# Kernel tuning notes

Hardware: AMD Instinct MI355X
Metric: run time of the kernel (lower is better)

## Reference

```python
import jax, jax.numpy as jnp
import numpy as np

BETA = 0.95
THR = 0.8
SLOPE = 25.0  # fast_sigmoid surrogate slope


@jax.custom_vjp
def spike(x):
    # Heaviside forward, fast-sigmoid surrogate backward (snntorch surrogate.fast_sigmoid)
    return (x > 0).astype(x.dtype)

def _spike_fwd(x):
    return spike(x), x

def _spike_bwd(x, g):
    return (g / (SLOPE * jnp.abs(x) + 1.0) ** 2,)

spike.defvjp(_spike_fwd, _spike_bwd)


def setup_inputs() -> dict:
    key = jax.random.key(0)
    k1, k2, k3 = jax.random.split(key, 3)
    B, T, D, H, C = 512, 2000, 20, 128, 10
    x = jax.random.normal(k1, (B, T, D), dtype=jnp.float32)
    # kaiming_normal_ with nonlinearity='linear': std = 1/sqrt(fan_in)
    W1 = jax.random.normal(k2, (H, D), dtype=jnp.float32) / np.sqrt(D)
    b1 = jnp.zeros((H,), jnp.float32)
    W2 = jax.random.normal(k3, (C, H), dtype=jnp.float32) / np.sqrt(H)
    b2 = jnp.zeros((C,), jnp.float32)
    return {"x": x, "W1": W1, "b1": b1, "W2": W2, "b2": b2}


def reference(x, W1, b1, W2, b2):
    B, T, D = x.shape
    H = W1.shape[0]

    def step(mem, xt):
        cur = xt @ W1.T + b1                                  # [B,H]
        # snntorch Leaky: reset based on PREVIOUS mem (detached), subtract mechanism
        reset = jax.lax.stop_gradient(spike(mem - THR))
        mem_new = BETA * mem + cur - reset * THR
        spk = spike(mem_new - THR)
        return mem_new, spk

    mem0 = jnp.zeros((B, H), x.dtype)
    _, spks = jax.lax.scan(step, mem0, jnp.swapaxes(x, 0, 1))  # spks: [T,B,H]

    spikeCounts = spks.sum(0)                                  # [B,H]
    # sum_t fc2(spk_t) = spikeCounts @ W2^T + T * b2
    logits = (spikeCounts @ W2.T + T * b2) / T
    logits = logits + 0.1 * ((spikeCounts / (T + 1e-6)) @ W2.T + b2)
    return logits
```

## Files before the change

kernel.cpp:

```cpp
#include <hip/hip_runtime.h>
#include <stdint.h>

#define Bdim 512
#define Tdim 2000
#define Ddim 20
#define Hdim 128
#define Cdim 10
#define TT   64
#define NCH  32
#define BETA 0.95f
#define THR  0.8f

typedef float f32x2 __attribute__((ext_vector_type(2)));
typedef float f32x4 __attribute__((ext_vector_type(4)));
typedef int   i32x4 __attribute__((ext_vector_type(4)));

#define CVT_HILO(HI, LO, F0, F1) {                                                     \
    asm volatile("v_cvt_pk_bf16_f32 %0, %1, %2" : "=v"(HI) : "v"(F0), "v"(F1));        \
    const float h0f_ = __uint_as_float((HI) << 16);                                    \
    const float h1f_ = __uint_as_float((HI) & 0xFFFF0000u);                            \
    const float l0_ = (F0) - h0f_;  const float l1_ = (F1) - h1f_;                     \
    asm volatile("v_cvt_pk_bf16_f32 %0, %1, %2" : "=v"(LO) : "v"(l0_), "v"(l1_)); }

#define MFMA0(ACC, A8, B8) \
  asm volatile("v_mfma_f32_16x16x32_bf16 %0, %1, %2, 0"  : "=v"(ACC) : "v"(A8), "v"(B8));
#define MFMA(ACC, A8, B8)  \
  asm volatile("v_mfma_f32_16x16x32_bf16 %0, %1, %2, %0" : "+v"(ACC) : "v"(A8), "v"(B8));

__global__ __launch_bounds__(256, 1) void snn_spec2_kernel(
    const float* __restrict__ x,
    const float* __restrict__ W1,
    const float* __restrict__ b1,
    const float* __restrict__ W2,
    const float* __restrict__ b2,
    float* __restrict__ out)
{
  const int b   = blockIdx.x;
  const int tid = threadIdx.x;
  const int wid = tid >> 6;
  const int l   = tid & 63;
  const int r   = l & 15;
  const int g   = l >> 4;

  __shared__ __align__(16) float xraw[2][TT * Ddim];
  __shared__ __align__(16) float cur[2][TT * 132];
  __shared__ float cnt_s[Hdim];

  const float* xb = x + (size_t)b * (Tdim * Ddim);
  const float* const clampMax = x + (size_t)Bdim * Tdim * Ddim - 4;

  const uint32_t xrawB = (uint32_t)(uintptr_t)&xraw[0][0];
  const uint32_t curB  = (uint32_t)(uintptr_t)&cur[0][0];

  i32x4 bhi[8], blo[8];
  f32x4 zero4, ovr;
  bool  sel23 = false, g3f = false;
  if (wid < 2) {
    const bool g2 = (g == 2);
    g3f   = (g == 3);
    sel23 = g2 | g3f;
    zero4[0]=0.f; zero4[1]=0.f; zero4[2]=0.f; zero4[3]=0.f;
    ovr = zero4; if (g2) ovr[0] = 1.0f;
#pragma unroll
    for (int ni = 0; ni < 8; ++ni) {
      const int hh = ni * 16 + r;
      float wv[8];
#pragma unroll
      for (int j = 0; j < 8; ++j) {
        const int k = 8 * g + j;
        wv[j] = (k < Ddim) ? W1[hh * Ddim + k] : ((k == Ddim) ? b1[hh] : 0.0f);
      }
#pragma unroll
      for (int d = 0; d < 4; ++d) {
        const uint32_t u0 = __float_as_uint(wv[2*d]), u1 = __float_as_uint(wv[2*d+1]);
        const uint32_t h0 = (u0 + 0x8000u) & 0xFFFF0000u;
        const uint32_t h1 = (u1 + 0x8000u) & 0xFFFF0000u;
        bhi[ni][d] = (int)(h1 | (h0 >> 16));
        const float l0 = wv[2*d]   - __uint_as_float(h0);
        const float l1 = wv[2*d+1] - __uint_as_float(h1);
        const uint32_t e0 = (__float_as_uint(l0) + 0x8000u) & 0xFFFF0000u;
        const uint32_t e1 = (__float_as_uint(l1) + 0x8000u) & 0xFFFF0000u;
        blo[ni][d] = (int)(e1 | (e0 >> 16));
      }
    }
  }

  float    mem = 0.0f;
  bool     sp  = false;
  uint32_t cnt = 0u;
  f32x2    negT2; negT2[0] = -THR; negT2[1] = -THR;
  const int sid = wid - 2;

#define STAGE(CH, BUF) do {                                                            \
    const float* g0_ = xb + (CH) * 1280 + wid * 640 + l * 4;                           \
    char* lb_ = (char*)&xraw[0][0] + (BUF) * 5120 + wid * 2560 + l * 16;               \
    const float* p0_ = g0_;        if (p0_ > clampMax) p0_ = clampMax;                 \
    const float* p1_ = g0_ + 256;  if (p1_ > clampMax) p1_ = clampMax;                 \
    __builtin_amdgcn_global_load_lds(                                                  \
      (const __attribute__((address_space(1))) unsigned int*)p0_,                      \
      (__attribute__((address_space(3))) unsigned int*)lb_, 16, 0, 0);                 \
    __builtin_amdgcn_global_load_lds(                                                  \
      (const __attribute__((address_space(1))) unsigned int*)p1_,                      \
      (__attribute__((address_space(3))) unsigned int*)(lb_ + 1024), 16, 0, 0);        \
    if (l < 32) {                                                                      \
      const float* p2_ = g0_ + 512;  if (p2_ > clampMax) p2_ = clampMax;               \
      __builtin_amdgcn_global_load_lds(                                                \
        (const __attribute__((address_space(1))) unsigned int*)p2_,                    \
        (__attribute__((address_space(3))) unsigned int*)(lb_ + 2048), 16, 0, 0);      \
    } } while (0)

#define CW2(NI, AC)                                                                    \
    asm volatile("ds_write2_b32 %0, %1, %2 offset0:%c3 offset1:%c4"                    \
                 :: "v"(cwb_),  "v"(AC[0]), "v"(AC[1]), "n"(16*(NI)), "n"(16*(NI)+132)); \
    asm volatile("ds_write2_b32 %0, %1, %2 offset0:%c3 offset1:%c4"                    \
                 :: "v"(cwb2_), "v"(AC[2]), "v"(AC[3]), "n"(16*(NI)), "n"(16*(NI)+132));

#define CWRM(MTIDX, P0,P1,P2,P3,P4,P5,P6,P7) {                                         \
    const uint32_t cwb_  = curB + (uint32_t)(pbuf * 33792 + 528 * ((MTIDX) * 16 + 4 * g) + 4 * r); \
    const uint32_t cwb2_ = cwb_ + 1056u;                                               \
    CW2(0,P0) CW2(1,P1) CW2(2,P2) CW2(3,P3) CW2(4,P4) CW2(5,P5) CW2(6,P6) CW2(7,P7) }

#define SELA(A0, A1) { A0 = g3f ? zero4 : A0;  A1 = sel23 ? ovr : A1; }

#define CVT8(AHI, ALO, A0, A1) {                                                       \
    uint32_t h_, lo_;                                                                  \
    CVT_HILO(h_, lo_, A0[0], A0[1]) AHI[0]=(int)h_; ALO[0]=(int)lo_;                   \
    CVT_HILO(h_, lo_, A0[2], A0[3]) AHI[1]=(int)h_; ALO[1]=(int)lo_;                   \
    CVT_HILO(h_, lo_, A1[0], A1[1]) AHI[2]=(int)h_; ALO[2]=(int)lo_;                   \
    CVT_HILO(h_, lo_, A1[2], A1[3]) AHI[3]=(int)h_; ALO[3]=(int)lo_; }

#define MM24(AHI, ALO, C0,C1,C2,C3,C4,C5,C6,C7)                                        \
    MFMA0(C0, ALO, bhi[0]) MFMA0(C1, ALO, bhi[1]) MFMA0(C2, ALO, bhi[2])               \
    MFMA0(C3, ALO, bhi[3]) MFMA0(C4, ALO, bhi[4]) MFMA0(C5, ALO, bhi[5])               \
    MFMA0(C6, ALO, bhi[6]) MFMA0(C7, ALO, bhi[7])                                      \
    MFMA (C0, AHI, blo[0]) MFMA (C1, AHI, blo[1]) MFMA (C2, AHI, blo[2])               \
    MFMA (C3, AHI, blo[3]) MFMA (C4, AHI, blo[4]) MFMA (C5, AHI, blo[5])               \
    MFMA (C6, AHI, blo[6]) MFMA (C7, AHI, blo[7])                                      \
    MFMA (C0, AHI, bhi[0]) MFMA (C1, AHI, bhi[1]) MFMA (C2, AHI, bhi[2])               \
    MFMA (C3, AHI, bhi[3]) MFMA (C4, AHI, bhi[4]) MFMA (C5, AHI, bhi[5])               \
    MFMA (C6, AHI, bhi[6]) MFMA (C7, AHI, bhi[7])

#define GEMM2() {                                                                      \
    const uint32_t afb_ = xrawB + (uint32_t)(pbuf * 5120 + (2*wid) * 1280 + 80 * r + 32 * g); \
    f32x4 a00_, a01_, a10_, a11_;                                                      \
    asm volatile("ds_read_b128 %0, %1 offset:0"    : "=v"(a00_) : "v"(afb_));          \
    asm volatile("ds_read_b128 %0, %1 offset:16"   : "=v"(a01_) : "v"(afb_));          \
    asm volatile("ds_read_b128 %0, %1 offset:1280" : "=v"(a10_) : "v"(afb_));          \
    asm volatile("ds_read_b128 %0, %1 offset:1296" : "=v"(a11_) : "v"(afb_));          \
    asm volatile("s_waitcnt lgkmcnt(2)" ::: "memory");                                 \
    __builtin_amdgcn_sched_barrier(0);                                                 \
    SELA(a00_, a01_)                                                                   \
    i32x4 ahi0_, alo0_;  CVT8(ahi0_, alo0_, a00_, a01_)                                \
    asm volatile("s_nop 2");                                                           \
    f32x4 c00,c01,c02,c03,c04,c05,c06,c07;                                             \
    MM24(ahi0_, alo0_, c00,c01,c02,c03,c04,c05,c06,c07)                                \
    asm volatile("s_waitcnt lgkmcnt(0)" ::: "memory");                                 \
    __builtin_amdgcn_sched_barrier(0);                                                 \
    SELA(a10_, a11_)                                                                   \
    i32x4 ahi1_, alo1_;  CVT8(ahi1_, alo1_, a10_, a11_)                                \
    asm volatile("s_nop 2");                                                           \
    f32x4 c10,c11,c12,c13,c14,c15,c16,c17;                                             \
    MM24(ahi1_, alo1_, c10,c11,c12,c13,c14,c15,c16,c17)                                \
    asm volatile("s_nop 7"); asm volatile("s_nop 4");                                  \
    CWRM(2*wid,     c00,c01,c02,c03,c04,c05,c06,c07)                                   \
    CWRM(2*wid + 1, c10,c11,c12,c13,c14,c15,c16,c17) }

#define GEMM_TAIL() {                                                                  \
    const uint32_t afb_ = xrawB + (uint32_t)(pbuf * 5120 + 80 * r + 32 * g);           \
    f32x4 a00_, a01_;                                                                  \
    asm volatile("ds_read_b128 %0, %1 offset:0"  : "=v"(a00_) : "v"(afb_));            \
    asm volatile("ds_read_b128 %0, %1 offset:16" : "=v"(a01_) : "v"(afb_));            \
    asm volatile("s_waitcnt lgkmcnt(0)" ::: "memory");                                 \
    __builtin_amdgcn_sched_barrier(0);                                                 \
    SELA(a00_, a01_)                                                                   \
    i32x4 ahi0_, alo0_;  CVT8(ahi0_, alo0_, a00_, a01_)                                \
    asm volatile("s_nop 2");                                                           \
    f32x4 c00,c01,c02,c03,c04,c05,c06,c07;                                             \
    MM24(ahi0_, alo0_, c00,c01,c02,c03,c04,c05,c06,c07)                                \
    asm volatile("s_nop 7"); asm volatile("s_nop 4");                                  \
    CWRM(0, c00,c01,c02,c03,c04,c05,c06,c07) }

#define RD2(PR, AD) asm volatile("ds_read2_b32 %0, %1 offset0:0 offset1:132" : "=v"(PR) : "v"(AD));
#define LGW(N) asm volatile("s_waitcnt lgkmcnt(" #N ")" ::: "memory"); __builtin_amdgcn_sched_barrier(0);
#define CONSUME(PR) {                                                                  \
    f32x2 cm_; asm("v_pk_add_f32 %0, %1, %2" : "=v"(cm_) : "v"(PR), "v"(negT2));       \
    float mP_ = fmaf(BETA, mem, PR[0]);                                                \
    float mM_ = fmaf(BETA, mem, cm_[0]);                                               \
    mem = sp ? mM_ : mP_;                                                              \
    sp  = mem > THR;                                                                   \
    cnt += sp ? 1u : 0u;                                                               \
    mP_ = fmaf(BETA, mem, PR[1]);                                                      \
    mM_ = fmaf(BETA, mem, cm_[1]);                                                     \
    mem = sp ? mM_ : mP_;                                                              \
    sp  = mem > THR;                                                                   \
    cnt += sp ? 1u : 0u; }
#define SSLOT(S) { LGW(7) CONSUME(pr##S) a##S += 8448u; RD2(pr##S, a##S) }
#define TSLOT(S, W) { LGW(W) CONSUME(pr##S) }
#define SCAN_PRO()                                                                     \
    uint32_t a0 = spB, a1 = spB+1056u, a2 = spB+2112u, a3 = spB+3168u,                 \
             a4 = spB+4224u, a5 = spB+5280u, a6 = spB+6336u, a7 = spB+7392u;           \
    f32x2 pr0, pr1, pr2, pr3, pr4, pr5, pr6, pr7;                                      \
    RD2(pr0,a0) RD2(pr1,a1) RD2(pr2,a2) RD2(pr3,a3)                                    \
    RD2(pr4,a4) RD2(pr5,a5) RD2(pr6,a6) RD2(pr7,a7)
#define SCAN_TAIL8()                                                                   \
    TSLOT(0,7) TSLOT(1,6) TSLOT(2,5) TSLOT(3,4)                                        \
    TSLOT(4,3) TSLOT(5,2) TSLOT(6,1) TSLOT(7,0)

  if (wid < 2) STAGE(0, 0);

#pragma unroll 1
  for (int ph = 0; ph <= NCH; ++ph) {
    if (wid < 2) {
      if (ph <= NCH - 1) {
        asm volatile("s_waitcnt vmcnt(0)" ::: "memory");
        if (ph < NCH - 1) STAGE(ph + 1, (ph + 1) & 1);
        const int pbuf = ph & 1;
        if (ph < NCH - 1) {
          GEMM2()
        } else if (wid == 0) {
          GEMM_TAIL()
        }
        asm volatile("s_waitcnt lgkmcnt(0)" ::: "memory");
      }
    } else {
      if (ph >= 1) {
        const uint32_t spB = curB + (uint32_t)(((ph - 1) & 1) * 33792 + 4 * (sid * 64 + l));
        if (ph - 1 < NCH - 1) {
          SCAN_PRO()
          SSLOT(0) SSLOT(1) SSLOT(2) SSLOT(3) SSLOT(4) SSLOT(5) SSLOT(6) SSLOT(7)
          SSLOT(0) SSLOT(1) SSLOT(2) SSLOT(3) SSLOT(4) SSLOT(5) SSLOT(6) SSLOT(7)
          SSLOT(0) SSLOT(1) SSLOT(2) SSLOT(3) SSLOT(4) SSLOT(5) SSLOT(6) SSLOT(7)
          SCAN_TAIL8()
        } else {
          SCAN_PRO()
          SCAN_TAIL8()
        }
        if (ph == NCH) cnt_s[sid * 64 + l] = (float)cnt;
      }
    }
    __builtin_amdgcn_sched_barrier(0);
    __builtin_amdgcn_s_barrier();
    __builtin_amdgcn_sched_barrier(0);
  }

  __syncthreads();

  if (tid < Cdim) {
    float dot = 0.0f;
#pragma unroll
    for (int k = 0; k < Hdim; ++k)
      dot = fmaf(cnt_s[k], W2[tid * Hdim + k], dot);
    const float Tf = (float)Tdim;
    const float scale = 1.0f / Tf + 0.1f / (Tf + 1e-6f);
    out[b * Cdim + tid] = fmaf(dot, scale, 1.1f * b2[tid]);
  }
}

extern "C" void kernel_launch(void* const* d_in, const int* in_sizes, int n_in,
                              void* d_out, int out_size, void* d_ws, size_t ws_size,
                              hipStream_t stream) {
  const float* x  = (const float*)d_in[0];
  const float* W1 = (const float*)d_in[1];
  const float* b1 = (const float*)d_in[2];
  const float* W2 = (const float*)d_in[3];
  const float* b2 = (const float*)d_in[4];
  float* out = (float*)d_out;

  snn_spec2_kernel<<<dim3(Bdim), dim3(256), 0, stream>>>(x, W1, b1, W2, b2, out);
}
```

Before: 62.50 us.

## Transpose cur buffer to hidden-major layout with b128 LDS access and asm scan

Changes the shared cur buffer from time-major [T][132] to hidden-major [H][66], so each MFMA accumulator tile is stored with one ds_write_b128 and each scan lane reads four consecutive timesteps with ds_read_b128 instead of ds_read2_b32 pairs. The scan recurrence is rewritten as inline asm that uses v_cmp/v_cndmask/v_addc to carry the spike flag and count through VCC. The goal is fewer LDS instructions and a shorter dependent chain in the serial scan. The risks are bank conflicts with the 264-byte row stride and extra VGPR pressure from holding six 4-wide prefetch buffers.

New measurement: 122.8 us. 1.96x slower.

```diff
diff --git a/kernel.cpp b/kernel.cpp
--- a/kernel.cpp
+++ b/kernel.cpp
@@ -27,7 +27,7 @@
 #define MFMA(ACC, A8, B8)  \
   asm volatile("v_mfma_f32_16x16x32_bf16 %0, %1, %2, %0" : "+v"(ACC) : "v"(A8), "v"(B8));
 
-__global__ __launch_bounds__(256, 1) void snn_spec2_kernel(
+__global__ __launch_bounds__(256, 1) void snn_spec3_kernel(
     const float* __restrict__ x,
     const float* __restrict__ W1,
     const float* __restrict__ b1,
@@ -43,7 +43,7 @@
   const int g   = l >> 4;
 
   __shared__ __align__(16) float xraw[2][TT * Ddim];
-  __shared__ __align__(16) float cur[2][TT * 132];
+  __shared__ __align__(16) float cur[2][Hdim * 66];
   __shared__ float cnt_s[Hdim];
 
   const float* xb = x + (size_t)b * (Tdim * Ddim);
@@ -86,9 +86,9 @@
   }
 
   float    mem = 0.0f;
-  bool     sp  = false;
   uint32_t cnt = 0u;
   f32x2    negT2; negT2[0] = -THR; negT2[1] = -THR;
+  float    betaV = BETA, thrV = THR;
   const int sid = wid - 2;
 
 #define STAGE(CH, BUF) do {                                                            \
@@ -109,19 +109,11 @@
         (__attribute__((address_space(3))) unsigned int*)(lb_ + 2048), 16, 0, 0);      \
     } } while (0)
 
-#define CW2(NI, AC)                                                                    \
-    asm volatile("ds_write2_b32 %0, %1, %2 offset0:%c3 offset1:%c4"                    \
-                 :: "v"(cwb_),  "v"(AC[0]), "v"(AC[1]), "n"(16*(NI)), "n"(16*(NI)+132)); \
-    asm volatile("ds_write2_b32 %0, %1, %2 offset0:%c3 offset1:%c4"                    \
-                 :: "v"(cwb2_), "v"(AC[2]), "v"(AC[3]), "n"(16*(NI)), "n"(16*(NI)+132));
-
-#define CWRM(MTIDX, P0,P1,P2,P3,P4,P5,P6,P7) {                                         \
-    const uint32_t cwb_  = curB + (uint32_t)(pbuf * 33792 + 528 * ((MTIDX) * 16 + 4 * g) + 4 * r); \
-    const uint32_t cwb2_ = cwb_ + 1056u;                                               \
-    CW2(0,P0) CW2(1,P1) CW2(2,P2) CW2(3,P3) CW2(4,P4) CW2(5,P5) CW2(6,P6) CW2(7,P7) }
+#define VM0()  asm volatile("s_waitcnt vmcnt(0)" ::: "memory");
+#define LGW(N) asm volatile("s_waitcnt lgkmcnt(" #N ")" ::: "memory"); __builtin_amdgcn_sched_barrier(0);
+#define BAR()  __builtin_amdgcn_sched_barrier(0); __builtin_amdgcn_s_barrier(); __builtin_amdgcn_sched_barrier(0);
 
 #define SELA(A0, A1) { A0 = g3f ? zero4 : A0;  A1 = sel23 ? ovr : A1; }
-
 #define CVT8(AHI, ALO, A0, A1) {                                                       \
     uint32_t h_, lo_;                                                                  \
     CVT_HILO(h_, lo_, A0[0], A0[1]) AHI[0]=(int)h_; ALO[0]=(int)lo_;                   \
@@ -140,71 +132,121 @@
     MFMA (C3, AHI, bhi[3]) MFMA (C4, AHI, bhi[4]) MFMA (C5, AHI, bhi[5])               \
     MFMA (C6, AHI, bhi[6]) MFMA (C7, AHI, bhi[7])
 
+#define WQ(CWB, AC, NI) \
+    asm volatile("ds_write_b128 %0, %1 offset:%c2" :: "v"(CWB), "v"(AC), "n"(4224*(NI)));
+#define WTILE(CWB, P0,P1,P2,P3,P4,P5,P6,P7)                                            \
+    WQ(CWB,P0,0) WQ(CWB,P1,1) WQ(CWB,P2,2) WQ(CWB,P3,3)                                \
+    WQ(CWB,P4,4) WQ(CWB,P5,5) WQ(CWB,P6,6) WQ(CWB,P7,7)
+
 #define GEMM2() {                                                                      \
-    const uint32_t afb_ = xrawB + (uint32_t)(pbuf * 5120 + (2*wid) * 1280 + 80 * r + 32 * g); \
+    const uint32_t afb_ = afb0 + pb * 5120u;                                           \
     f32x4 a00_, a01_, a10_, a11_;                                                      \
     asm volatile("ds_read_b128 %0, %1 offset:0"    : "=v"(a00_) : "v"(afb_));          \
     asm volatile("ds_read_b128 %0, %1 offset:16"   : "=v"(a01_) : "v"(afb_));          \
     asm volatile("ds_read_b128 %0, %1 offset:1280" : "=v"(a10_) : "v"(afb_));          \
     asm volatile("ds_read_b128 %0, %1 offset:1296" : "=v"(a11_) : "v"(afb_));          \
-    asm volatile("s_waitcnt lgkmcnt(2)" ::: "memory");                                 \
-    __builtin_amdgcn_sched_barrier(0);                                                 \
+    LGW(2)                                                                             \
     SELA(a00_, a01_)                                                                   \
     i32x4 ahi0_, alo0_;  CVT8(ahi0_, alo0_, a00_, a01_)                                \
     asm volatile("s_nop 2");                                                           \
     f32x4 c00,c01,c02,c03,c04,c05,c06,c07;                                             \
     MM24(ahi0_, alo0_, c00,c01,c02,c03,c04,c05,c06,c07)                                \
-    asm volatile("s_waitcnt lgkmcnt(0)" ::: "memory");                                 \
-    __builtin_amdgcn_sched_barrier(0);                                                 \
+    LGW(0)                                                                             \
     SELA(a10_, a11_)                                                                   \
     i32x4 ahi1_, alo1_;  CVT8(ahi1_, alo1_, a10_, a11_)                                \
     asm volatile("s_nop 2");                                                           \
     f32x4 c10,c11,c12,c13,c14,c15,c16,c17;                                             \
     MM24(ahi1_, alo1_, c10,c11,c12,c13,c14,c15,c16,c17)                                \
     asm volatile("s_nop 7"); asm volatile("s_nop 4");                                  \
-    CWRM(2*wid,     c00,c01,c02,c03,c04,c05,c06,c07)                                   \
-    CWRM(2*wid + 1, c10,c11,c12,c13,c14,c15,c16,c17) }
+    const uint32_t cw0_ = cwb0 + pb * 33792u;                                          \
+    WTILE(cw0_,       c00,c01,c02,c03,c04,c05,c06,c07)                                 \
+    WTILE(cw0_ + 64u, c10,c11,c12,c13,c14,c15,c16,c17) }
 
 #define GEMM_TAIL() {                                                                  \
-    const uint32_t afb_ = xrawB + (uint32_t)(pbuf * 5120 + 80 * r + 32 * g);           \
+    const uint32_t afb_ = afb0 + pb * 5120u;                                           \
     f32x4 a00_, a01_;                                                                  \
     asm volatile("ds_read_b128 %0, %1 offset:0"  : "=v"(a00_) : "v"(afb_));            \
     asm volatile("ds_read_b128 %0, %1 offset:16" : "=v"(a01_) : "v"(afb_));            \
-    asm volatile("s_waitcnt lgkmcnt(0)" ::: "memory");                                 \
-    __builtin_amdgcn_sched_barrier(0);                                                 \
+    LGW(0)                                                                             \
     SELA(a00_, a01_)                                                                   \
     i32x4 ahi0_, alo0_;  CVT8(ahi0_, alo0_, a00_, a01_)                                \
     asm volatile("s_nop 2");                                                           \
     f32x4 c00,c01,c02,c03,c04,c05,c06,c07;                                             \
     MM24(ahi0_, alo0_, c00,c01,c02,c03,c04,c05,c06,c07)                                \
     asm volatile("s_nop 7"); asm volatile("s_nop 4");                                  \
-    CWRM(0, c00,c01,c02,c03,c04,c05,c06,c07) }
-
-#define RD2(PR, AD) asm volatile("ds_read2_b32 %0, %1 offset0:0 offset1:132" : "=v"(PR) : "v"(AD));
-#define LGW(N) asm volatile("s_waitcnt lgkmcnt(" #N ")" ::: "memory"); __builtin_amdgcn_sched_barrier(0);
-#define CONSUME(PR) {                                                                  \
-    f32x2 cm_; asm("v_pk_add_f32 %0, %1, %2" : "=v"(cm_) : "v"(PR), "v"(negT2));       \
-    float mP_ = fmaf(BETA, mem, PR[0]);                                                \
-    float mM_ = fmaf(BETA, mem, cm_[0]);                                               \
-    mem = sp ? mM_ : mP_;                                                              \
-    sp  = mem > THR;                                                                   \
-    cnt += sp ? 1u : 0u;                                                               \
-    mP_ = fmaf(BETA, mem, PR[1]);                                                      \
-    mM_ = fmaf(BETA, mem, cm_[1]);                                                     \
-    mem = sp ? mM_ : mP_;                                                              \
-    sp  = mem > THR;                                                                   \
-    cnt += sp ? 1u : 0u; }
-#define SSLOT(S) { LGW(7) CONSUME(pr##S) a##S += 8448u; RD2(pr##S, a##S) }
-#define TSLOT(S, W) { LGW(W) CONSUME(pr##S) }
-#define SCAN_PRO()                                                                     \
-    uint32_t a0 = spB, a1 = spB+1056u, a2 = spB+2112u, a3 = spB+3168u,                 \
-             a4 = spB+4224u, a5 = spB+5280u, a6 = spB+6336u, a7 = spB+7392u;           \
-    f32x2 pr0, pr1, pr2, pr3, pr4, pr5, pr6, pr7;                                      \
-    RD2(pr0,a0) RD2(pr1,a1) RD2(pr2,a2) RD2(pr3,a3)                                    \
-    RD2(pr4,a4) RD2(pr5,a5) RD2(pr6,a6) RD2(pr7,a7)
-#define SCAN_TAIL8()                                                                   \
-    TSLOT(0,7) TSLOT(1,6) TSLOT(2,5) TSLOT(3,4)                                        \
-    TSLOT(4,3) TSLOT(5,2) TSLOT(6,1) TSLOT(7,0)
+    const uint32_t cwt_ = curB + pb * 33792u + 264u * (uint32_t)r + 16u * (uint32_t)g; \
+    WTILE(cwt_, c00,c01,c02,c03,c04,c05,c06,c07) }
+
+#define RDQ(Q, AD, OFF) \
+    asm volatile("ds_read_b128 %0, %1 offset:%c2" : "=v"(Q) : "v"(AD), "n"(OFF));
+
+#define SCAN_SLOT(PR) {                                                                \
+    f32x2 a01_; a01_[0] = PR[0]; a01_[1] = PR[1];                                      \
+    f32x2 a23_; a23_[0] = PR[2]; a23_[1] = PR[3];                                      \
+    f32x2 cm01_, cm23_;                                                                \
+    asm("v_pk_add_f32 %0, %1, %2" : "=v"(cm01_) : "v"(a01_), "v"(negT2));              \
+    asm("v_pk_add_f32 %0, %1, %2" : "=v"(cm23_) : "v"(a23_), "v"(negT2));              \
+    float t0_, t1_;  uint64_t j_;                                                      \
+    asm volatile(                                                                      \
+      "v_cmp_lt_f32 vcc, %[TH], %[mem]\n\t"                                            \
+      "v_fma_f32 %[t0], %[bt], %[mem], %[c0]\n\t"                                      \
+      "v_fma_f32 %[t1], %[bt], %[mem], %[m0]\n\t"                                      \
+      "v_cndmask_b32 %[mem], %[t0], %[t1], vcc\n\t"                                    \
+      "v_cmp_lt_f32 vcc, %[TH], %[mem]\n\t"                                            \
+      "v_addc_co_u32 %[cnt], %[jj], %[cnt], 0, vcc\n\t"                                \
+      "v_fma_f32 %[t0], %[bt], %[mem], %[c1]\n\t"                                      \
+      "v_fma_f32 %[t1], %[bt], %[mem], %[m1]\n\t"                                      \
+      "v_cndmask_b32 %[mem], %[t0], %[t1], vcc\n\t"                                    \
+      "v_cmp_lt_f32 vcc, %[TH], %[mem]\n\t"                                            \
+      "v_addc_co_u32 %[cnt], %[jj], %[cnt], 0, vcc\n\t"                                \
+      "v_fma_f32 %[t0], %[bt], %[mem], %[c2]\n\t"                                      \
+      "v_fma_f32 %[t1], %[bt], %[mem], %[m2]\n\t"                                      \
+      "v_cndmask_b32 %[mem], %[t0], %[t1], vcc\n\t"                                    \
+      "v_cmp_lt_f32 vcc, %[TH], %[mem]\n\t"                                            \
+      "v_addc_co_u32 %[cnt], %[jj], %[cnt], 0, vcc\n\t"                                \
+      "v_fma_f32 %[t0], %[bt], %[mem], %[c3]\n\t"                                      \
+      "v_fma_f32 %[t1], %[bt], %[mem], %[m3]\n\t"                                      \
+      "v_cndmask_b32 %[mem], %[t0], %[t1], vcc\n\t"                                    \
+      "v_cmp_lt_f32 vcc, %[TH], %[mem]\n\t"                                            \
+      "v_addc_co_u32 %[cnt], %[jj], %[cnt], 0, vcc"                                    \
+      : [mem]"+v"(mem), [cnt]"+v"(cnt), [t0]"=&v"(t0_), [t1]"=&v"(t1_), [jj]"=s"(j_)   \
+      : [bt]"v"(betaV), [TH]"v"(thrV),                                                 \
+        [c0]"v"(PR[0]), [c1]"v"(PR[1]), [c2]"v"(PR[2]), [c3]"v"(PR[3]),                \
+        [m0]"v"(cm01_[0]), [m1]"v"(cm01_[1]), [m2]"v"(cm23_[0]), [m3]"v"(cm23_[1])     \
+      : "vcc"); }
+
+#define SCAN_FULL(SPB) {                                                               \
+    f32x4 q0,q1,q2,q3,q4,q5;                                                           \
+    RDQ(q0,SPB,0) RDQ(q1,SPB,16) RDQ(q2,SPB,32) RDQ(q3,SPB,48)                         \
+    RDQ(q4,SPB,64) RDQ(q5,SPB,80)                                                      \
+    LGW(5) SCAN_SLOT(q0) RDQ(q0,SPB,96)                                                \
+    LGW(5) SCAN_SLOT(q1) RDQ(q1,SPB,112)                                               \
+    LGW(5) SCAN_SLOT(q2) RDQ(q2,SPB,128)                                               \
+    LGW(5) SCAN_SLOT(q3) RDQ(q3,SPB,144)                                               \
+    LGW(5) SCAN_SLOT(q4) RDQ(q4,SPB,160)                                               \
+    LGW(5) SCAN_SLOT(q5) RDQ(q5,SPB,176)                                               \
+    LGW(5) SCAN_SLOT(q0) RDQ(q0,SPB,192)                                               \
+    LGW(5) SCAN_SLOT(q1) RDQ(q1,SPB,208)                                               \
+    LGW(5) SCAN_SLOT(q2) RDQ(q2,SPB,224)                                               \
+    LGW(5) SCAN_SLOT(q3) RDQ(q3,SPB,240)                                               \
+    LGW(5) SCAN_SLOT(q4)                                                               \
+    LGW(4) SCAN_SLOT(q5)                                                               \
+    LGW(3) SCAN_SLOT(q0)                                                               \
+    LGW(2) SCAN_SLOT(q1)                                                               \
+    LGW(1) SCAN_SLOT(q2)                                                               \
+    LGW(0) SCAN_SLOT(q3) }
+
+#define SCAN_TAIL(SPB) {                                                               \
+    f32x4 q0,q1,q2,q3;                                                                 \
+    RDQ(q0,SPB,0) RDQ(q1,SPB,16) RDQ(q2,SPB,32) RDQ(q3,SPB,48)                         \
+    LGW(3) SCAN_SLOT(q0)                                                               \
+    LGW(2) SCAN_SLOT(q1)                                                               \
+    LGW(1) SCAN_SLOT(q2)                                                               \
+    LGW(0) SCAN_SLOT(q3) }
+
+  const uint32_t afb0 = xrawB + (uint32_t)(2560 * wid + 80 * r + 32 * g);
+  const uint32_t cwb0 = curB + (uint32_t)(264 * r + 128 * wid + 16 * g);
+  const uint32_t spB0 = curB + (uint32_t)((sid * 64 + l) * 264);
 
   if (wid < 2) STAGE(0, 0);
 
@@ -212,35 +254,25 @@
   for (int ph = 0; ph <= NCH; ++ph) {
     if (wid < 2) {
       if (ph <= NCH - 1) {
-        asm volatile("s_waitcnt vmcnt(0)" ::: "memory");
+        VM0()
         if (ph < NCH - 1) STAGE(ph + 1, (ph + 1) & 1);
-        const int pbuf = ph & 1;
+        const uint32_t pb = (uint32_t)(ph & 1);
         if (ph < NCH - 1) {
           GEMM2()
         } else if (wid == 0) {
           GEMM_TAIL()
         }
-        asm volatile("s_waitcnt lgkmcnt(0)" ::: "memory");
+        LGW(0)
       }
     } else {
       if (ph >= 1) {
-        const uint32_t spB = curB + (uint32_t)(((ph - 1) & 1) * 33792 + 4 * (sid * 64 + l));
-        if (ph - 1 < NCH - 1) {
-          SCAN_PRO()
-          SSLOT(0) SSLOT(1) SSLOT(2) SSLOT(3) SSLOT(4) SSLOT(5) SSLOT(6) SSLOT(7)
-          SSLOT(0) SSLOT(1) SSLOT(2) SSLOT(3) SSLOT(4) SSLOT(5) SSLOT(6) SSLOT(7)
-          SSLOT(0) SSLOT(1) SSLOT(2) SSLOT(3) SSLOT(4) SSLOT(5) SSLOT(6) SSLOT(7)
-          SCAN_TAIL8()
-        } else {
-          SCAN_PRO()
-          SCAN_TAIL8()
-        }
+        const uint32_t spB = spB0 + (uint32_t)(((ph - 1) & 1) * 33792);
+        if (ph - 1 < NCH - 1) { SCAN_FULL(spB) }
+        else                  { SCAN_TAIL(spB) }
         if (ph == NCH) cnt_s[sid * 64 + l] = (float)cnt;
       }
     }
-    __builtin_amdgcn_sched_barrier(0);
-    __builtin_amdgcn_s_barrier();
-    __builtin_amdgcn_sched_barrier(0);
+    BAR()
   }
 
   __syncthreads();
@@ -266,5 +298,5 @@
   const float* b2 = (const float*)d_in[4];
   float* out = (float*)d_out;
 
-  snn_spec2_kernel<<<dim3(Bdim), dim3(256), 0, stream>>>(x, W1, b1, W2, b2, out);
+  snn_spec3_kernel<<<dim3(Bdim), dim3(256), 0, stream>>>(x, W1, b1, W2, b2, out);
 }
```
